# Performance work log

Hardware: AMD Instinct MI355X
Metric: run time of the kernel (lower is better)

The kernel has to match this reference:

```python
import jax, jax.numpy as jnp
import numpy as np

B, T, D, H = 2, 2048, 1024, 16
HD = D // H
DFF = 4 * D
EPS = 1e-5


def gelu_tanh(x):
    c = jnp.sqrt(2.0 / jnp.pi).astype(x.dtype)
    return 0.5 * x * (1.0 + jnp.tanh(c * (x + 0.044715 * x ** 3)))


def layernorm(x, scale, shift):
    mean = jnp.mean(x, axis=-1, keepdims=True)
    var = jnp.var(x, axis=-1, keepdims=True)  # unbiased=False
    return (x - mean) / jnp.sqrt(var + EPS) * scale + shift


def setup_inputs() -> dict:
    key = jax.random.key(0)
    ks = jax.random.split(key, 12)
    s = lambda fan_in: 1.0 / np.sqrt(fan_in)
    return {
        "x": jax.random.normal(ks[0], (B, T, D), jnp.float32),
        "wq": jax.random.normal(ks[1], (D, D), jnp.float32) * s(D),
        "wk": jax.random.normal(ks[2], (D, D), jnp.float32) * s(D),
        "wv": jax.random.normal(ks[3], (D, D), jnp.float32) * s(D),
        "wo": jax.random.normal(ks[4], (D, D), jnp.float32) * s(D),
        "bo": jnp.zeros((D,), jnp.float32),
        "ln1_scale": jnp.ones((D,), jnp.float32),
        "ln1_shift": jnp.zeros((D,), jnp.float32),
        "ln2_scale": jnp.ones((D,), jnp.float32),
        "ln2_shift": jnp.zeros((D,), jnp.float32),
        "w1": jax.random.normal(ks[5], (D, DFF), jnp.float32) * s(D),
        "b1": jnp.zeros((DFF,), jnp.float32),
        "w2": jax.random.normal(ks[6], (DFF, D), jnp.float32) * s(DFF),
        "b2": jnp.zeros((D,), jnp.float32),
    }


def reference(x, wq, wk, wv, wo, bo, ln1_scale, ln1_shift, ln2_scale, ln2_shift, w1, b1, w2, b2):
    # pre-LN attention
    h = layernorm(x, ln1_scale, ln1_shift)
    q = (h @ wq).reshape(B, T, H, HD).transpose(0, 2, 1, 3)  # [B,H,T,hd]
    k = (h @ wk).reshape(B, T, H, HD).transpose(0, 2, 1, 3)
    v = (h @ wv).reshape(B, T, H, HD).transpose(0, 2, 1, 3)
    scores = jnp.einsum('bhqd,bhkd->bhqk', q, k) / jnp.sqrt(jnp.float32(HD))
    causal = jnp.tril(jnp.ones((T, T), bool))
    scores = jnp.where(causal, scores, -jnp.inf)
    attn = jax.nn.softmax(scores, axis=-1)
    ctx = jnp.einsum('bhqk,bhkd->bhqd', attn, v)
    ctx = ctx.transpose(0, 2, 1, 3).reshape(B, T, D)
    attn_out = ctx @ wo + bo
    x = x + attn_out  # dropout p=0
    # pre-LN FFN
    h2 = layernorm(x, ln2_scale, ln2_shift)
    ff = gelu_tanh(h2 @ w1 + b1) @ w2 + b2
    return x + ff
```

## Files before the change

### kernel.cpp

```cpp
#include <hip/hip_runtime.h>
#include <hip/hip_bf16.h>
#include <stdint.h>

typedef unsigned short u16;
typedef __attribute__((ext_vector_type(8))) short s16x8;
typedef __attribute__((ext_vector_type(4))) float f32x4;

#define B_   2
#define T_   2048
#define D_   1024
#define H_   16
#define HD_  64
#define DFF_ 4096
#define M_   (B_*T_)

#define SC2F 0.18033688f

__device__ __forceinline__ u16 f2b(float f){
  uint32_t u = __float_as_uint(f);
  u += 0x7FFFu + ((u >> 16) & 1u);
  return (u16)(u >> 16);
}
__device__ __forceinline__ float b2f(u16 u){ return __uint_as_float(((uint32_t)u) << 16); }
__device__ __forceinline__ uint32_t pk2(float lo, float hi){
  uint32_t r;
  asm volatile("v_cvt_pk_bf16_f32 %0, %1, %2" : "=v"(r) : "v"(lo), "v"(hi));
  return r;
}

__device__ __forceinline__ void gl_lds16(const void* g, void* l){
  __builtin_amdgcn_global_load_lds((const __attribute__((address_space(1))) void*)g,
                                   (__attribute__((address_space(3))) void*)l, 16, 0, 0);
}

template<int N> __device__ __forceinline__ void waitvm(){
  if constexpr (N == 0)      asm volatile("s_waitcnt vmcnt(0)" ::: "memory");
  else if constexpr (N == 2) asm volatile("s_waitcnt vmcnt(2)" ::: "memory");
  else                       asm volatile("s_waitcnt vmcnt(4)" ::: "memory");
}

__global__ __launch_bounds__(256) void wconv_all(const float* __restrict__ wq,
                                                 const float* __restrict__ wk,
                                                 const float* __restrict__ wv,
                                                 const float* __restrict__ wo,
                                                 const float* __restrict__ w1,
                                                 const float* __restrict__ w2,
                                                 u16* __restrict__ wqkvT, u16* __restrict__ woT,
                                                 u16* __restrict__ w1T,   u16* __restrict__ w2T,
                                                 const float* __restrict__ x,
                                                 const float* __restrict__ ln1s,
                                                 const float* __restrict__ ln1b,
                                                 u16* __restrict__ hout){
  const int bid = blockIdx.x;
  const int tid = threadIdx.x;
  if (bid >= 3072){
    const int row = bid - 3072;
    float4 a = reinterpret_cast<const float4*>(x + ((size_t)row << 10))[tid];
    float s = a.x + a.y + a.z + a.w;
    float q = a.x*a.x + a.y*a.y + a.z*a.z + a.w*a.w;
    #pragma unroll
    for (int o = 32; o > 0; o >>= 1){ s += __shfl_xor(s, o); q += __shfl_xor(q, o); }
    __shared__ float red[8];
    const int w = tid >> 6;
    if ((tid & 63) == 0){ red[w] = s; red[4 + w] = q; }
    __syncthreads();
    float S = red[0] + red[1] + red[2] + red[3];
    float Q = red[4] + red[5] + red[6] + red[7];
    float mean = S * (1.0f/1024.0f);
    float var  = Q * (1.0f/1024.0f) - mean*mean;
    float inv = rsqrtf(var + 1e-5f);
    float4 gsc = reinterpret_cast<const float4*>(ln1s)[tid];
    float4 gsh = reinterpret_cast<const float4*>(ln1b)[tid];
    ushort4 o4;
    o4.x = f2b((a.x - mean)*inv*gsc.x + gsh.x);
    o4.y = f2b((a.y - mean)*inv*gsc.y + gsh.y);
    o4.z = f2b((a.z - mean)*inv*gsc.z + gsh.z);
    o4.w = f2b((a.w - mean)*inv*gsc.w + gsh.w);
    reinterpret_cast<ushort4*>(hout + ((size_t)row << 10))[tid] = o4;
    return;
  }
  const float* W; u16* Wt; int K, N, tk, tn;
  if (bid < 1024){
    const int which = bid >> 8, t = bid & 255; tk = t >> 4; tn = t & 15; K = 1024; N = 1024;
    W  = (which == 0) ? wq : (which == 1) ? wk : (which == 2) ? wv : wo;
    Wt = (which == 3) ? woT : wqkvT + (size_t)which * D_ * D_;
  } else if (bid < 2048){
    const int t = bid - 1024; tk = t >> 6; tn = t & 63; K = 1024; N = 4096; W = w1; Wt = w1T;
  } else {
    const int t = bid - 2048; tk = t >> 4; tn = t & 15; K = 4096; N = 1024; W = w2; Wt = w2T;
  }
  const int k0 = tk << 6, n0 = tn << 6;
  __shared__ u16 tile[64][68];
  const int rr = tid >> 4, c4 = (tid & 15) << 2;
  #pragma unroll
  for (int rep = 0; rep < 4; rep++){
    int r = rr + (rep << 4);
    float4 v = *reinterpret_cast<const float4*>(W + (size_t)(k0 + r)*N + n0 + c4);
    tile[r][c4+0] = f2b(v.x); tile[r][c4+1] = f2b(v.y);
    tile[r][c4+2] = f2b(v.z); tile[r][c4+3] = f2b(v.w);
  }
  __syncthreads();
  const int rn = tid >> 2, kb = (tid & 3) << 4;
  u16 tmp[16];
  #pragma unroll
  for (int j = 0; j < 16; j++) tmp[j] = tile[kb + j][rn];
  ushort4* dst = reinterpret_cast<ushort4*>(Wt + (size_t)(n0 + rn)*K + k0 + kb);
  dst[0] = make_ushort4(tmp[0], tmp[1], tmp[2], tmp[3]);
  dst[1] = make_ushort4(tmp[4], tmp[5], tmp[6], tmp[7]);
  dst[2] = make_ushort4(tmp[8], tmp[9], tmp[10], tmp[11]);
  dst[3] = make_ushort4(tmp[12], tmp[13], tmp[14], tmp[15]);
}

__global__ __launch_bounds__(256) void reduce2(const u16* __restrict__ p,
                                               const float* __restrict__ bias,
                                               const float* __restrict__ resid,
                                               float* __restrict__ out){
  const size_t idx = ((size_t)blockIdx.x << 8) + threadIdx.x;
  ushort4 a4 = reinterpret_cast<const ushort4*>(p)[idx];
  ushort4 b4 = reinterpret_cast<const ushort4*>(p)[idx + (((size_t)M_*D_) >> 2)];
  float4 r = reinterpret_cast<const float4*>(resid)[idx];
  float4 bb = reinterpret_cast<const float4*>(bias)[threadIdx.x];
  float4 o;
  o.x = b2f(a4.x) + b2f(b4.x) + r.x + bb.x;
  o.y = b2f(a4.y) + b2f(b4.y) + r.y + bb.y;
  o.z = b2f(a4.z) + b2f(b4.z) + r.z + bb.z;
  o.w = b2f(a4.w) + b2f(b4.w) + r.w + bb.w;
  reinterpret_cast<float4*>(out)[idx] = o;
}

__global__ __launch_bounds__(256) void reduce_ln(const u16* __restrict__ p,
                                                 const float* __restrict__ bias,
                                                 const float* __restrict__ resid,
                                                 const float* __restrict__ sc,
                                                 const float* __restrict__ sh,
                                                 float* __restrict__ x1,
                                                 u16* __restrict__ h2){
  const int row = blockIdx.x;
  const int tid = threadIdx.x;
  const size_t idx = ((size_t)row << 8) + tid;
  ushort4 a4 = reinterpret_cast<const ushort4*>(p)[idx];
  ushort4 b4 = reinterpret_cast<const ushort4*>(p)[idx + (((size_t)M_*D_) >> 2)];
  float4 r  = reinterpret_cast<const float4*>(resid)[idx];
  float4 bb = reinterpret_cast<const float4*>(bias)[tid];
  float4 v;
  v.x = b2f(a4.x) + b2f(b4.x) + r.x + bb.x;
  v.y = b2f(a4.y) + b2f(b4.y) + r.y + bb.y;
  v.z = b2f(a4.z) + b2f(b4.z) + r.z + bb.z;
  v.w = b2f(a4.w) + b2f(b4.w) + r.w + bb.w;
  reinterpret_cast<float4*>(x1)[idx] = v;
  float s = v.x + v.y + v.z + v.w;
  float q = v.x*v.x + v.y*v.y + v.z*v.z + v.w*v.w;
  #pragma unroll
  for (int o = 32; o > 0; o >>= 1){ s += __shfl_xor(s, o); q += __shfl_xor(q, o); }
  __shared__ float red[8];
  const int w = tid >> 6;
  if ((tid & 63) == 0){ red[w] = s; red[4 + w] = q; }
  __syncthreads();
  float S = red[0] + red[1] + red[2] + red[3];
  float Q = red[4] + red[5] + red[6] + red[7];
  float mean = S * (1.0f/1024.0f);
  float var  = Q * (1.0f/1024.0f) - mean*mean;
  float inv = rsqrtf(var + 1e-5f);
  float4 gsc = reinterpret_cast<const float4*>(sc)[tid];
  float4 gsh = reinterpret_cast<const float4*>(sh)[tid];
  ushort4 o4;
  o4.x = f2b((v.x - mean)*inv*gsc.x + gsh.x);
  o4.y = f2b((v.y - mean)*inv*gsc.y + gsh.y);
  o4.z = f2b((v.z - mean)*inv*gsc.z + gsh.z);
  o4.w = f2b((v.w - mean)*inv*gsc.w + gsh.w);
  reinterpret_cast<ushort4*>(h2 + ((size_t)row << 10))[tid] = o4;
}

template<int EPI, int NF>
__global__ __launch_bounds__(512, 2) void gemm8(const u16* __restrict__ A, const u16* __restrict__ Bt,
                                                const float* __restrict__ bias,
                                                void* __restrict__ Cv, void* __restrict__ Cv2,
                                                int M, int N, int K, int lda){
  constexpr int BROWS = NF * 32;
  __shared__ __align__(16) u16 LA[2][2][128*64];
  __shared__ __align__(16) u16 LB[2][2][BROWS*64];
  const int tid = threadIdx.x;
  const int lane = tid & 63;
  const int w = tid >> 6;
  const int wm = w >> 2, wn = w & 3;
  const int g = lane >> 4, l15 = lane & 15;
  const int bnb = (wn & 1) * (NF * 16);

  const int nx = gridDim.x, ny = gridDim.y;
  const int nwg = nx * ny * gridDim.z;
  const int flat = blockIdx.x + nx * (blockIdx.y + ny * blockIdx.z);
  const int nfid = (flat & 7) * (nwg >> 3) + (flat >> 3);
  const int tn = nfid % nx;
  const int rest = nfid / nx;
  const int tm = rest % ny;
  const int kz = rest / ny;
  const int tn0 = tn * (NF * 64);
  const int tm0 = tm << 8;
  const u16* Az = A  + (size_t)kz * K;
  const u16* Bz = Bt + (size_t)kz * K;

  const int arow0 = tid >> 3,         asl0 = (((tid) & 7) ^ (arow0 & 7)) << 3;
  const int arow1 = (tid + 512) >> 3, asl1 = (((tid + 512) & 7) ^ (arow1 & 7)) << 3;

  f32x4 acc[8][NF];
  #pragma unroll
  for (int i = 0; i < 8; i++)
    #pragma unroll
    for (int j = 0; j < NF; j++) acc[i][j] = (f32x4){0.f,0.f,0.f,0.f};
  s16x8 bf[NF][2];

#define STG_A(db, h, tt) do{                                                        \
    gl_lds16(Az + (size_t)(tm0 + (h)*128 + arow0)*lda + ((tt) << 6) + asl0,         \
             &LA[db][h][tid*8]);                                                    \
    gl_lds16(Az + (size_t)(tm0 + (h)*128 + arow1)*lda + ((tt) << 6) + asl1,         \
             &LA[db][h][(tid + 512)*8]);                                            \
  }while(0)
#define STG_B(db, h, tt) do{                                                        \
    gl_lds16(Bz + (size_t)(tn0 + (h)*BROWS + arow0)*lda + ((tt) << 6) + asl0,       \
             &LB[db][h][tid*8]);                                                    \
    if constexpr (NF == 4){                                                         \
      gl_lds16(Bz + (size_t)(tn0 + (h)*BROWS + arow1)*lda + ((tt) << 6) + asl1,     \
               &LB[db][h][(tid + 512)*8]);                                          \
    }                                                                               \
  }while(0)
#define LDAF(db, mf, kk) (*reinterpret_cast<const s16x8*>(                          \
    &LA[db][wm][((mf)*16 + l15)*64 + ((((kk)*4 + g) ^ (l15 & 7)) << 3)]))
#define LDBF(db, nf, kk) (*reinterpret_cast<const s16x8*>(                          \
    &LB[db][wn >> 1][(bnb + (nf)*16 + l15)*64 + ((((kk)*4 + g) ^ (l15 & 7)) << 3)]))
#define BLOAD(db) do{ _Pragma("unroll")                                             \
    for (int nf = 0; nf < NF; nf++){ bf[nf][0] = LDBF(db, nf, 0);                   \
                                     bf[nf][1] = LDBF(db, nf, 1); } }while(0)
#define PH(db, MFA, MFB, STG, WV) do{                                               \
    s16x8 a00 = LDAF(db, MFA, 0), a01 = LDAF(db, MFA, 1);                           \
    s16x8 a10 = LDAF(db, MFB, 0), a11 = LDAF(db, MFB, 1);                           \
    STG;                                                                            \
    WV;                                                                             \
    __builtin_amdgcn_s_barrier();                                                   \
    __builtin_amdgcn_s_setprio(1);                                                  \
    _Pragma("unroll")                                                               \
    for (int nf = 0; nf < NF; nf++){                                                \
      acc[MFA][nf] = __builtin_amdgcn_mfma_f32_16x16x32_bf16(a00, bf[nf][0], acc[MFA][nf], 0,0,0); \
      acc[MFA][nf] = __builtin_amdgcn_mfma_f32_16x16x32_bf16(a01, bf[nf][1], acc[MFA][nf], 0,0,0); \
      acc[MFB][nf] = __builtin_amdgcn_mfma_f32_16x16x32_bf16(a10, bf[nf][0], acc[MFB][nf], 0,0,0); \
      acc[MFB][nf] = __builtin_amdgcn_mfma_f32_16x16x32_bf16(a11, bf[nf][1], acc[MFB][nf], 0,0,0); \
    }                                                                               \
    __builtin_amdgcn_s_setprio(0);                                                  \
    __builtin_amdgcn_s_barrier();                                                   \
  }while(0)

  const int NT = K >> 6;
  STG_B(0, 0, 0); STG_B(0, 1, 0); STG_A(0, 0, 0); STG_A(0, 1, 0);
  STG_B(1, 0, 1); STG_B(1, 1, 1);
  waitvm<NF>();
  __builtin_amdgcn_s_barrier();

  for (int t = 0; t < NT; t += 2){
    const bool last = (t + 2 >= NT);
    BLOAD(0);
    PH(0, 0, 1, STG_A(1, 0, t + 1), );
    PH(0, 2, 3, STG_A(1, 1, t + 1), );
    PH(0, 4, 5, if (!last) STG_B(0, 0, t + 2), );
    PH(0, 6, 7, if (!last) STG_B(0, 1, t + 2),
                if (last) waitvm<0>(); else waitvm<NF>(););
    BLOAD(1);
    PH(1, 0, 1, if (!last) STG_A(0, 0, t + 2), );
    PH(1, 2, 3, if (!last) STG_A(0, 1, t + 2), );
    PH(1, 4, 5, if (!last) STG_B(1, 0, t + 3), );
    PH(1, 6, 7, if (!last) STG_B(1, 1, t + 3),
                if (last) waitvm<0>(); else waitvm<NF>(););
  }
#undef STG_A
#undef STG_B
#undef LDAF
#undef LDBF
#undef BLOAD
#undef PH

  if constexpr (EPI == 1){
    const int sel = tn0 >> 10;
    if (sel < 2){
      #pragma unroll
      for (int mf = 0; mf < 8; mf++){
        const int mb = tm0 + wm*128 + mf*16 + (g << 2);
        #pragma unroll
        for (int nf = 0; nf < NF; nf++){
          const int n = tn0 + wn*(NF*16) + nf*16 + l15;
          const int nn = n & 1023;
          const int hh = nn >> 6, d = nn & 63;
          #pragma unroll
          for (int rr = 0; rr < 4; rr++){
            const int m = mb + rr;
            float v = acc[mf][nf][rr];
            if (sel == 0) v *= SC2F;
            ((u16*)Cv)[(size_t)sel*((size_t)M_*D_) +
                       ((((size_t)(m >> 11)*H_ + hh)*T_ + (m & 2047)) << 6) + d] = f2b(v);
          }
        }
      }
    } else {
      u16* TR = &LA[0][0][0];
      u16* vt = (u16*)Cv2;
      const int bq = tm0 >> 11;
      const int tloc = tm0 & 2047;
      #pragma unroll
      for (int hp = 0; hp < 2; hp++){
        __syncthreads();
        if ((wn >> 1) == hp){
          #pragma unroll
          for (int mf = 0; mf < 8; mf++){
            const int mb = wm*128 + mf*16 + (g << 2);
            #pragma unroll
            for (int nf = 0; nf < NF; nf++){
              const int nr = ((wn & 1) << 6) + (nf << 4) + l15;
              #pragma unroll
              for (int rr = 0; rr < 4; rr++){
                const int m = mb + rr;
                TR[nr*256 + (((m >> 3) ^ (nr & 15)) << 3) + (m & 7)] = f2b(acc[mf][nf][rr]);
              }
            }
          }
        }
        __syncthreads();
        {
          const int nr = tid >> 2;
          const int m0 = (tid & 3) << 6;
          const int nn = (tn0 & 1023) + (hp << 7) + nr;
          const int hh = nn >> 6, d = nn & 63;
          u16* dst = vt + (((size_t)(bq*H_ + hh))*HD_ + d)*T_ + tloc + m0;
          #pragma unroll
          for (int jj = 0; jj < 8; jj++){
            const int j = (m0 >> 3) + jj;
            s16x8 vv = *reinterpret_cast<const s16x8*>(&TR[nr*256 + ((j ^ (nr & 15)) << 3)]);
            *reinterpret_cast<s16x8*>(dst + jj*8) = vv;
          }
        }
      }
    }
  } else {
    #pragma unroll
    for (int mf = 0; mf < 8; mf++){
      const int mb = tm0 + wm*128 + mf*16 + (g << 2);
      #pragma unroll
      for (int nf = 0; nf < NF; nf++){
        const int n = tn0 + wn*(NF*16) + nf*16 + l15;
        #pragma unroll
        for (int rr = 0; rr < 4; rr++){
          const int m = mb + rr;
          float v = acc[mf][nf][rr];
          if constexpr (EPI == 0){
            ((u16*)Cv)[(size_t)kz*((size_t)M*N) + (size_t)m*N + n] = f2b(v);
          } else {
            float u = v + bias[n];
            float t2 = 0.7978845608f*(u + 0.044715f*u*u*u);
            float e = __expf(2.0f*t2);
            float th = 1.0f - 2.0f/(e + 1.0f);
            ((u16*)Cv)[(size_t)m*N + n] = f2b(0.5f*u*(1.0f + th));
          }
        }
      }
    }
  }
}

__global__ __launch_bounds__(512) void attn_k(const u16* __restrict__ Qg, const u16* __restrict__ Kg,
                                              const u16* __restrict__ Vg, u16* __restrict__ ctx){
  const int flat = blockIdx.x + (blockIdx.y << 3);
  const int xcd = flat & 7, j_ = (flat >> 3) & 3, pr_ = flat >> 5;
  const int bh  = (j_ << 3) + xcd;
  const int tid = threadIdx.x;
  const int lane = tid & 63;
  const int w = tid >> 6;
  const int g = lane >> 4, l15 = lane & 15;

  __shared__ __align__(16) u16 Qs[128*64];
  __shared__ __align__(16) u16 Ks[2][128*64];
  __shared__ __align__(16) u16 Vt[2][64*128];
  __shared__ __align__(16) u16 Pl[8][16*128];
  u16* const Plw = &Pl[w][0];

  const size_t hb = (size_t)bh * ((size_t)T_*HD_);
  const u16* Qh = Qg + hb;
  const u16* Kh = Kg + hb;
  const u16* Vh = Vg + hb;
  const int b = bh >> 4, hh = bh & 15;

  const int qk_r0 = tid >> 3,         qk_c0 = (((tid) & 7) ^ (qk_r0 & 7)) << 3;
  const int qk_r1 = (tid + 512) >> 3, qk_c1 = (((tid + 512) & 7) ^ (qk_r1 & 7)) << 3;
  const int v_r0 = tid >> 4,          v_c0 = (((tid) & 15) ^ (v_r0 & 7)) << 3;
  const int v_r1 = (tid + 512) >> 4,  v_c1 = (((tid + 512) & 15) ^ (v_r1 & 7)) << 3;

  for (int ph = 0; ph < 2; ++ph){
    const int qt = ph ? (15 - pr_) : pr_;
    const int NKT = qt + 1;

    gl_lds16(Qh + (size_t)(qt*128 + qk_r0)*HD_ + qk_c0, Qs + tid*8);
    gl_lds16(Qh + (size_t)(qt*128 + qk_r1)*HD_ + qk_c1, Qs + (tid+512)*8);
    gl_lds16(Kh + (size_t)qk_r0*HD_ + qk_c0, Ks[0] + tid*8);
    gl_lds16(Kh + (size_t)qk_r1*HD_ + qk_c1, Ks[0] + (tid+512)*8);
    gl_lds16(Vh + (size_t)v_r0*T_ + v_c0, Vt[0] + tid*8);
    gl_lds16(Vh + (size_t)v_r1*T_ + v_c1, Vt[0] + (tid+512)*8);
    __syncthreads();

    s16x8 qa[2];
    #pragma unroll
    for (int kk = 0; kk < 2; kk++){
      int ra = (w << 4) + l15;
      int slot = (kk << 2) + g;
      qa[kk] = *reinterpret_cast<const s16x8*>(Qs + ra*64 + ((slot ^ (ra & 7)) << 3));
    }

    f32x4 accO[4];
    #pragma unroll
    for (int j = 0; j < 4; j++) accO[j] = (f32x4){0.f,0.f,0.f,0.f};
    float mrow = -1e30f, lrow = 0.f;
    const int qgl = qt*128 + (w << 4) + l15;

    for (int kt = 0; kt < NKT; ++kt){
      const int cur = kt & 1, nxt = cur ^ 1;
      const bool pf = (kt + 1 < NKT);

      if (pf){
        gl_lds16(Kh + (size_t)((kt+1)*128 + qk_r0)*HD_ + qk_c0, Ks[nxt] + tid*8);
        gl_lds16(Kh + (size_t)((kt+1)*128 + qk_r1)*HD_ + qk_c1, Ks[nxt] + (tid+512)*8);
        gl_lds16(Vh + (size_t)v_r0*T_ + (kt+1)*128 + v_c0, Vt[nxt] + tid*8);
        gl_lds16(Vh + (size_t)v_r1*T_ + (kt+1)*128 + v_c1, Vt[nxt] + (tid+512)*8);
      }

      f32x4 accS[8];
      #pragma unroll
      for (int j = 0; j < 8; j++) accS[j] = (f32x4){0.f,0.f,0.f,0.f};
      __builtin_amdgcn_s_setprio(1);
      #pragma unroll
      for (int jn = 0; jn < 8; jn++){
        #pragma unroll
        for (int kk = 0; kk < 2; kk++){
          int rb = (jn << 4) + l15;
          int slot = (kk << 2) + g;
          s16x8 kf = *reinterpret_cast<const s16x8*>(Ks[cur] + rb*64 + ((slot ^ (rb & 7)) << 3));
          accS[jn] = __builtin_amdgcn_mfma_f32_16x16x32_bf16(kf, qa[kk], accS[jn], 0, 0, 0);
        }
      }
      __builtin_amdgcn_s_setprio(0);

      if (kt == qt){
        #pragma unroll
        for (int jn = 0; jn < 8; jn++)
          #pragma unroll
          for (int rr = 0; rr < 4; rr++){
            int kgl = kt*128 + (jn << 4) + (g << 2) + rr;
            if (kgl > qgl) accS[jn][rr] = -1e30f;
          }
      }

      float rmax = accS[0][0];
      #pragma unroll
      for (int jn = 0; jn < 8; jn++)
        #pragma unroll
        for (int rr = 0; rr < 4; rr++) rmax = fmaxf(rmax, accS[jn][rr]);
      rmax = fmaxf(rmax, __shfl_xor(rmax, 16));
      rmax = fmaxf(rmax, __shfl_xor(rmax, 32));

      if (__any(rmax > mrow + 8.0f)){
        float mn = fmaxf(mrow, rmax);
        float sf = exp2f(mrow - mn);
        mrow = mn;
        lrow *= sf;
        #pragma unroll
        for (int rr = 0; rr < 4; rr++){
          float sfr = __shfl(sf, ((lane >> 4) << 2) + rr);
          #pragma unroll
          for (int jn = 0; jn < 4; jn++) accO[jn][rr] *= sfr;
        }
      }

      float tsum = 0.f;
      #pragma unroll
      for (int jn = 0; jn < 8; jn++){
        float pv0 = exp2f(accS[jn][0] - mrow);
        float pv1 = exp2f(accS[jn][1] - mrow);
        float pv2 = exp2f(accS[jn][2] - mrow);
        float pv3 = exp2f(accS[jn][3] - mrow);
        tsum += (pv0 + pv1) + (pv2 + pv3);
        int ch = ((jn << 1) | (g >> 1)) ^ (l15 & 7);
        int base = (l15 << 7) + (ch << 3) + ((g & 1) << 2);
        uint2 pkd = make_uint2(pk2(pv0, pv1), pk2(pv2, pv3));
        *reinterpret_cast<uint2*>(&Plw[base]) = pkd;
      }
      tsum += __shfl_xor(tsum, 16);
      tsum += __shfl_xor(tsum, 32);
      lrow += tsum;

      __builtin_amdgcn_s_setprio(1);
      #pragma unroll
      for (int kk = 0; kk < 4; kk++){
        int pch = ((kk << 2) + g) ^ (l15 & 7);
        s16x8 pa = *reinterpret_cast<const s16x8*>(&Plw[(l15 << 7) + (pch << 3)]);
        #pragma unroll
        for (int jn = 0; jn < 4; jn++){
          int vd = (jn << 4) + l15;
          int vslot = (((kk << 2) + g) & 8) | ((((kk << 2) + g) ^ (vd & 7)) & 7);
          s16x8 vbf = *reinterpret_cast<const s16x8*>(Vt[cur] + (vd << 7) + (vslot << 3));
          accO[jn] = __builtin_amdgcn_mfma_f32_16x16x32_bf16(pa, vbf, accO[jn], 0, 0, 0);
        }
      }
      __builtin_amdgcn_s_setprio(0);

      __syncthreads();
    }

    #pragma unroll
    for (int rr = 0; rr < 4; rr++){
      float lr = __shfl(lrow, ((lane >> 4) << 2) + rr);
      float inv = 1.0f / lr;
      int qrow = qt*128 + (w << 4) + (g << 2) + rr;
      size_t rowbase = ((size_t)(b*T_ + qrow) << 10) + ((size_t)hh << 6);
      #pragma unroll
      for (int jn = 0; jn < 4; jn++){
        int d = (jn << 4) + l15;
        ctx[rowbase + d] = f2b(accO[jn][rr] * inv);
      }
    }
  }
}

extern "C" void kernel_launch(void* const* d_in, const int* in_sizes, int n_in,
                              void* d_out, int out_size, void* d_ws, size_t ws_size,
                              hipStream_t stream){
  (void)in_sizes; (void)n_in; (void)out_size; (void)ws_size;
  const float* x    = (const float*)d_in[0];
  const float* wq   = (const float*)d_in[1];
  const float* wk   = (const float*)d_in[2];
  const float* wv   = (const float*)d_in[3];
  const float* wo   = (const float*)d_in[4];
  const float* bo   = (const float*)d_in[5];
  const float* ln1s = (const float*)d_in[6];
  const float* ln1b = (const float*)d_in[7];
  const float* ln2s = (const float*)d_in[8];
  const float* ln2b = (const float*)d_in[9];
  const float* w1   = (const float*)d_in[10];
  const float* b1   = (const float*)d_in[11];
  const float* w2   = (const float*)d_in[12];
  const float* b2   = (const float*)d_in[13];
  float* out = (float*)d_out;

  char* p = (char*)d_ws;
  u16*  wqkvT = (u16*)p;  p += (size_t)3*D_*D_*2;
  u16*  woT   = (u16*)p;  p += (size_t)D_*D_*2;
  u16*  w1T   = (u16*)p;  p += (size_t)D_*DFF_*2;
  u16*  w2T   = (u16*)p;  p += (size_t)DFF_*D_*2;
  u16*  h     = (u16*)p;  p += (size_t)M_*D_*2;
  u16*  qb    = (u16*)p;  p += (size_t)M_*D_*2;
  u16*  kb    = (u16*)p;  p += (size_t)M_*D_*2;
  u16*  vb    = (u16*)p;  p += (size_t)M_*D_*2;
  u16*  ctx   = (u16*)p;  p += (size_t)M_*D_*2;
  float* x1   = (float*)p; p += (size_t)M_*D_*4;
  u16*  h2    = (u16*)p;  p += (size_t)M_*D_*2;
  u16*  ff1   = (u16*)p;  p += (size_t)M_*DFF_*2;
  (void)kb; (void)vb;
  u16* part = h;

  dim3 blk(256), blk8(512);
  wconv_all<<<3072 + M_, blk, 0, stream>>>(wq, wk, wv, wo, w1, w2, wqkvT, woT, w1T, w2T,
                                           x, ln1s, ln1b, h);
  gemm8<1,4><<<dim3(12,16,1), blk8, 0, stream>>>(h, wqkvT, nullptr, qb, ff1, M_, 3*D_, D_, D_);
  attn_k<<<dim3(8,32), blk8, 0, stream>>>(qb, qb + (size_t)M_*D_, ff1, ctx);
  gemm8<0,2><<<dim3(8,16,2), blk8, 0, stream>>>(ctx, woT, nullptr, part, nullptr, M_, D_, D_/2, D_);
  reduce_ln<<<M_, blk, 0, stream>>>(part, bo, x, ln2s, ln2b, x1, h2);
  gemm8<3,4><<<dim3(16,16,1), blk8, 0, stream>>>(h2, w1T, b1, ff1, nullptr, M_, DFF_, D_, D_);
  gemm8<0,2><<<dim3(8,16,2), blk8, 0, stream>>>(ff1, w2T, nullptr, part, nullptr, M_, D_, DFF_/2, DFF_);
  reduce2<<<M_, blk, 0, stream>>>(part, b2, x1, out);
}
```

Before: 221.1 us.

## Overlap w1/w2 conversion with QKV GEMM, store residual in bf16, tune waitcnt

The w1/w2 fp32-to-bf16 transposes move out of the initial conversion kernel and into extra blocks appended to the QKV GEMM launch, so they can run alongside the GEMM tiles. The intermediate residual x1 is stored as bf16 instead of fp32, which halves its write and read traffic in reduce_ln and reduce2 but adds rounding error to the residual path. The vmcnt wait threshold for NF=4 is raised from 4 to 8, allowing more loads in flight. The QKV GEMM now uses a hardcoded 1D tile mapping.

```diff
diff --git a/kernel.cpp b/kernel.cpp
--- a/kernel.cpp
+++ b/kernel.cpp
@@ -36,25 +36,47 @@
 template<int N> __device__ __forceinline__ void waitvm(){
   if constexpr (N == 0)      asm volatile("s_waitcnt vmcnt(0)" ::: "memory");
   else if constexpr (N == 2) asm volatile("s_waitcnt vmcnt(2)" ::: "memory");
-  else                       asm volatile("s_waitcnt vmcnt(4)" ::: "memory");
+  else if constexpr (N == 4) asm volatile("s_waitcnt vmcnt(4)" ::: "memory");
+  else                       asm volatile("s_waitcnt vmcnt(8)" ::: "memory");
+}
+
+__device__ __forceinline__ void wconv_tile(const float* __restrict__ W, u16* __restrict__ Wt,
+                                           int K, int N, int tk, int tn, int tid,
+                                           u16* __restrict__ tile ){
+  const int k0 = tk << 6, n0 = tn << 6;
+  const int rr = tid >> 4, c4 = (tid & 15) << 2;
+  #pragma unroll
+  for (int rep = 0; rep < 4; rep++){
+    int r = rr + (rep << 4);
+    float4 v = *reinterpret_cast<const float4*>(W + (size_t)(k0 + r)*N + n0 + c4);
+    tile[r*68 + c4+0] = f2b(v.x); tile[r*68 + c4+1] = f2b(v.y);
+    tile[r*68 + c4+2] = f2b(v.z); tile[r*68 + c4+3] = f2b(v.w);
+  }
+  __syncthreads();
+  const int rn = tid >> 2, kb = (tid & 3) << 4;
+  u16 tmp[16];
+  #pragma unroll
+  for (int j = 0; j < 16; j++) tmp[j] = tile[(kb + j)*68 + rn];
+  ushort4* dst = reinterpret_cast<ushort4*>(Wt + (size_t)(n0 + rn)*K + k0 + kb);
+  dst[0] = make_ushort4(tmp[0], tmp[1], tmp[2], tmp[3]);
+  dst[1] = make_ushort4(tmp[4], tmp[5], tmp[6], tmp[7]);
+  dst[2] = make_ushort4(tmp[8], tmp[9], tmp[10], tmp[11]);
+  dst[3] = make_ushort4(tmp[12], tmp[13], tmp[14], tmp[15]);
 }
 
 __global__ __launch_bounds__(256) void wconv_all(const float* __restrict__ wq,
                                                  const float* __restrict__ wk,
                                                  const float* __restrict__ wv,
                                                  const float* __restrict__ wo,
-                                                 const float* __restrict__ w1,
-                                                 const float* __restrict__ w2,
                                                  u16* __restrict__ wqkvT, u16* __restrict__ woT,
-                                                 u16* __restrict__ w1T,   u16* __restrict__ w2T,
                                                  const float* __restrict__ x,
                                                  const float* __restrict__ ln1s,
                                                  const float* __restrict__ ln1b,
                                                  u16* __restrict__ hout){
   const int bid = blockIdx.x;
   const int tid = threadIdx.x;
-  if (bid >= 3072){
-    const int row = bid - 3072;
+  if (bid >= 1024){
+    const int row = bid - 1024;
     float4 a = reinterpret_cast<const float4*>(x + ((size_t)row << 10))[tid];
     float s = a.x + a.y + a.z + a.w;
     float q = a.x*a.x + a.y*a.y + a.z*a.z + a.w*a.w;
@@ -79,52 +101,27 @@
     reinterpret_cast<ushort4*>(hout + ((size_t)row << 10))[tid] = o4;
     return;
   }
-  const float* W; u16* Wt; int K, N, tk, tn;
-  if (bid < 1024){
-    const int which = bid >> 8, t = bid & 255; tk = t >> 4; tn = t & 15; K = 1024; N = 1024;
-    W  = (which == 0) ? wq : (which == 1) ? wk : (which == 2) ? wv : wo;
-    Wt = (which == 3) ? woT : wqkvT + (size_t)which * D_ * D_;
-  } else if (bid < 2048){
-    const int t = bid - 1024; tk = t >> 6; tn = t & 63; K = 1024; N = 4096; W = w1; Wt = w1T;
-  } else {
-    const int t = bid - 2048; tk = t >> 4; tn = t & 15; K = 4096; N = 1024; W = w2; Wt = w2T;
-  }
-  const int k0 = tk << 6, n0 = tn << 6;
-  __shared__ u16 tile[64][68];
-  const int rr = tid >> 4, c4 = (tid & 15) << 2;
-  #pragma unroll
-  for (int rep = 0; rep < 4; rep++){
-    int r = rr + (rep << 4);
-    float4 v = *reinterpret_cast<const float4*>(W + (size_t)(k0 + r)*N + n0 + c4);
-    tile[r][c4+0] = f2b(v.x); tile[r][c4+1] = f2b(v.y);
-    tile[r][c4+2] = f2b(v.z); tile[r][c4+3] = f2b(v.w);
-  }
-  __syncthreads();
-  const int rn = tid >> 2, kb = (tid & 3) << 4;
-  u16 tmp[16];
-  #pragma unroll
-  for (int j = 0; j < 16; j++) tmp[j] = tile[kb + j][rn];
-  ushort4* dst = reinterpret_cast<ushort4*>(Wt + (size_t)(n0 + rn)*K + k0 + kb);
-  dst[0] = make_ushort4(tmp[0], tmp[1], tmp[2], tmp[3]);
-  dst[1] = make_ushort4(tmp[4], tmp[5], tmp[6], tmp[7]);
-  dst[2] = make_ushort4(tmp[8], tmp[9], tmp[10], tmp[11]);
-  dst[3] = make_ushort4(tmp[12], tmp[13], tmp[14], tmp[15]);
+  __shared__ u16 tile[64*68];
+  const int which = bid >> 8, t = bid & 255;
+  const float* W = (which == 0) ? wq : (which == 1) ? wk : (which == 2) ? wv : wo;
+  u16* Wt = (which == 3) ? woT : wqkvT + (size_t)which * D_ * D_;
+  wconv_tile(W, Wt, 1024, 1024, t >> 4, t & 15, tid, tile);
 }
 
 __global__ __launch_bounds__(256) void reduce2(const u16* __restrict__ p,
                                                const float* __restrict__ bias,
-                                               const float* __restrict__ resid,
+                                               const u16* __restrict__ resid,
                                                float* __restrict__ out){
   const size_t idx = ((size_t)blockIdx.x << 8) + threadIdx.x;
   ushort4 a4 = reinterpret_cast<const ushort4*>(p)[idx];
   ushort4 b4 = reinterpret_cast<const ushort4*>(p)[idx + (((size_t)M_*D_) >> 2)];
-  float4 r = reinterpret_cast<const float4*>(resid)[idx];
+  ushort4 r4 = reinterpret_cast<const ushort4*>(resid)[idx];
   float4 bb = reinterpret_cast<const float4*>(bias)[threadIdx.x];
   float4 o;
-  o.x = b2f(a4.x) + b2f(b4.x) + r.x + bb.x;
-  o.y = b2f(a4.y) + b2f(b4.y) + r.y + bb.y;
-  o.z = b2f(a4.z) + b2f(b4.z) + r.z + bb.z;
-  o.w = b2f(a4.w) + b2f(b4.w) + r.w + bb.w;
+  o.x = b2f(a4.x) + b2f(b4.x) + b2f(r4.x) + bb.x;
+  o.y = b2f(a4.y) + b2f(b4.y) + b2f(r4.y) + bb.y;
+  o.z = b2f(a4.z) + b2f(b4.z) + b2f(r4.z) + bb.z;
+  o.w = b2f(a4.w) + b2f(b4.w) + b2f(r4.w) + bb.w;
   reinterpret_cast<float4*>(out)[idx] = o;
 }
 
@@ -133,7 +130,7 @@
                                                  const float* __restrict__ resid,
                                                  const float* __restrict__ sc,
                                                  const float* __restrict__ sh,
-                                                 float* __restrict__ x1,
+                                                 u16* __restrict__ x1,
                                                  u16* __restrict__ h2){
   const int row = blockIdx.x;
   const int tid = threadIdx.x;
@@ -147,7 +144,9 @@
   v.y = b2f(a4.y) + b2f(b4.y) + r.y + bb.y;
   v.z = b2f(a4.z) + b2f(b4.z) + r.z + bb.z;
   v.w = b2f(a4.w) + b2f(b4.w) + r.w + bb.w;
-  reinterpret_cast<float4*>(x1)[idx] = v;
+  ushort4 xo;
+  xo.x = f2b(v.x); xo.y = f2b(v.y); xo.z = f2b(v.z); xo.w = f2b(v.w);
+  reinterpret_cast<ushort4*>(x1)[idx] = xo;
   float s = v.x + v.y + v.z + v.w;
   float q = v.x*v.x + v.y*v.y + v.z*v.z + v.w*v.w;
   #pragma unroll
@@ -175,25 +174,47 @@
 __global__ __launch_bounds__(512, 2) void gemm8(const u16* __restrict__ A, const u16* __restrict__ Bt,
                                                 const float* __restrict__ bias,
                                                 void* __restrict__ Cv, void* __restrict__ Cv2,
+                                                const float* __restrict__ cw1,
+                                                const float* __restrict__ cw2,
+                                                u16* __restrict__ w1T, u16* __restrict__ w2T,
                                                 int M, int N, int K, int lda){
   constexpr int BROWS = NF * 32;
   __shared__ __align__(16) u16 LA[2][2][128*64];
   __shared__ __align__(16) u16 LB[2][2][BROWS*64];
   const int tid = threadIdx.x;
+
+  if constexpr (EPI == 1){
+    if (blockIdx.x >= 192){
+      const int tid256 = tid & 255, sel2 = tid >> 8;
+      u16* tile = &LA[0][0][0] + sel2 * (64*68);
+      const int t = ((int)blockIdx.x - 192)*2 + sel2;
+      if (t < 1024) wconv_tile(cw1, w1T, 1024, 4096, t >> 6, t & 63, tid256, tile);
+      else          wconv_tile(cw2, w2T, 4096, 1024, (t-1024) >> 4, (t-1024) & 15, tid256, tile);
+      return;
+    }
+  }
+
   const int lane = tid & 63;
   const int w = tid >> 6;
   const int wm = w >> 2, wn = w & 3;
   const int g = lane >> 4, l15 = lane & 15;
   const int bnb = (wn & 1) * (NF * 16);
 
-  const int nx = gridDim.x, ny = gridDim.y;
-  const int nwg = nx * ny * gridDim.z;
-  const int flat = blockIdx.x + nx * (blockIdx.y + ny * blockIdx.z);
-  const int nfid = (flat & 7) * (nwg >> 3) + (flat >> 3);
-  const int tn = nfid % nx;
-  const int rest = nfid / nx;
-  const int tm = rest % ny;
-  const int kz = rest / ny;
+  int tn, tm, kz;
+  if constexpr (EPI == 1){
+    const int flat = blockIdx.x;
+    const int nfid = (flat & 7) * 24 + (flat >> 3);
+    tn = nfid % 12; tm = nfid / 12; kz = 0;
+  } else {
+    const int nx = gridDim.x, ny = gridDim.y;
+    const int nwg = nx * ny * gridDim.z;
+    const int flat = blockIdx.x + nx * (blockIdx.y + ny * blockIdx.z);
+    const int nfid = (flat & 7) * (nwg >> 3) + (flat >> 3);
+    tn = nfid % nx;
+    const int rest = nfid / nx;
+    tm = rest % ny;
+    kz = rest / ny;
+  }
   const int tn0 = tn * (NF * 64);
   const int tm0 = tm << 8;
   const u16* Az = A  + (size_t)kz * K;
@@ -208,6 +229,7 @@
     #pragma unroll
     for (int j = 0; j < NF; j++) acc[i][j] = (f32x4){0.f,0.f,0.f,0.f};
   s16x8 bf[NF][2];
+  constexpr int WVN = (NF == 4) ? 8 : 2;
 
 #define STG_A(db, h, tt) do{                                                        \
     gl_lds16(Az + (size_t)(tm0 + (h)*128 + arow0)*lda + ((tt) << 6) + asl0,         \
@@ -261,13 +283,13 @@
     PH(0, 2, 3, STG_A(1, 1, t + 1), );
     PH(0, 4, 5, if (!last) STG_B(0, 0, t + 2), );
     PH(0, 6, 7, if (!last) STG_B(0, 1, t + 2),
-                if (last) waitvm<0>(); else waitvm<NF>(););
+                if (last) waitvm<0>(); else waitvm<WVN>(););
     BLOAD(1);
     PH(1, 0, 1, if (!last) STG_A(0, 0, t + 2), );
     PH(1, 2, 3, if (!last) STG_A(0, 1, t + 2), );
     PH(1, 4, 5, if (!last) STG_B(1, 0, t + 3), );
     PH(1, 6, 7, if (!last) STG_B(1, 1, t + 3),
-                if (last) waitvm<0>(); else waitvm<NF>(););
+                if (last) waitvm<0>(); else waitvm<WVN>(););
   }
 #undef STG_A
 #undef STG_B
@@ -553,20 +575,26 @@
   u16*  kb    = (u16*)p;  p += (size_t)M_*D_*2;
   u16*  vb    = (u16*)p;  p += (size_t)M_*D_*2;
   u16*  ctx   = (u16*)p;  p += (size_t)M_*D_*2;
-  float* x1   = (float*)p; p += (size_t)M_*D_*4;
+  u16*  x1    = (u16*)p;  p += (size_t)M_*D_*2;
   u16*  h2    = (u16*)p;  p += (size_t)M_*D_*2;
   u16*  ff1   = (u16*)p;  p += (size_t)M_*DFF_*2;
   (void)kb; (void)vb;
   u16* part = h;
 
   dim3 blk(256), blk8(512);
-  wconv_all<<<3072 + M_, blk, 0, stream>>>(wq, wk, wv, wo, w1, w2, wqkvT, woT, w1T, w2T,
-                                           x, ln1s, ln1b, h);
-  gemm8<1,4><<<dim3(12,16,1), blk8, 0, stream>>>(h, wqkvT, nullptr, qb, ff1, M_, 3*D_, D_, D_);
+  wconv_all<<<1024 + M_, blk, 0, stream>>>(wq, wk, wv, wo, wqkvT, woT, x, ln1s, ln1b, h);
+  gemm8<1,4><<<192 + 1024, blk8, 0, stream>>>(h, wqkvT, nullptr, qb, ff1,
+                                              w1, w2, w1T, w2T, M_, 3*D_, D_, D_);
   attn_k<<<dim3(8,32), blk8, 0, stream>>>(qb, qb + (size_t)M_*D_, ff1, ctx);
-  gemm8<0,2><<<dim3(8,16,2), blk8, 0, stream>>>(ctx, woT, nullptr, part, nullptr, M_, D_, D_/2, D_);
+  gemm8<0,2><<<dim3(8,16,2), blk8, 0, stream>>>(ctx, woT, nullptr, part, nullptr,
+                                                nullptr, nullptr, nullptr, nullptr,
+                                                M_, D_, D_/2, D_);
   reduce_ln<<<M_, blk, 0, stream>>>(part, bo, x, ln2s, ln2b, x1, h2);
-  gemm8<3,4><<<dim3(16,16,1), blk8, 0, stream>>>(h2, w1T, b1, ff1, nullptr, M_, DFF_, D_, D_);
-  gemm8<0,2><<<dim3(8,16,2), blk8, 0, stream>>>(ff1, w2T, nullptr, part, nullptr, M_, D_, DFF_/2, DFF_);
+  gemm8<3,4><<<dim3(16,16,1), blk8, 0, stream>>>(h2, w1T, b1, ff1, nullptr,
+                                                 nullptr, nullptr, nullptr, nullptr,
+                                                 M_, DFF_, D_, D_);
+  gemm8<0,2><<<dim3(8,16,2), blk8, 0, stream>>>(ff1, w2T, nullptr, part, nullptr,
+                                                nullptr, nullptr, nullptr, nullptr,
+                                                M_, D_, DFF_/2, DFF_);
   reduce2<<<M_, blk, 0, stream>>>(part, b2, x1, out);
 }
```

After: 212.7 us. -3.8%, faster.
